# Kernel optimization log

Measured on AMD Instinct MI355X. Metric: run time of the kernel, lower is better.

The kernel has to match this reference:

```python
import jax, jax.numpy as jnp
import numpy as np

N = 100000
E = 6400000
H = 64  # hidden_nf


def setup_inputs() -> dict:
    key = jax.random.key(0)
    ks = jax.random.split(key, 12)
    x = jax.random.normal(ks[0], (N, 3), dtype=jnp.float32)
    vel = jax.random.normal(ks[1], (N, 3), dtype=jnp.float32)
    vel_norm = jax.random.uniform(ks[2], (N, 1), dtype=jnp.float32)
    edge_index = jax.random.randint(ks[3], (2, E), 0, N, dtype=jnp.int32)
    # coord_mlp_vel: Linear(1,H) -> LeakyReLU(0.2) -> Linear(H,1)
    W1 = jax.random.normal(ks[4], (H, 1), dtype=jnp.float32) * (1.0 / np.sqrt(1))
    b1 = jnp.zeros((H,), dtype=jnp.float32)
    W2 = jax.random.normal(ks[5], (1, H), dtype=jnp.float32) * (1.0 / np.sqrt(H))
    b2 = jnp.zeros((1,), dtype=jnp.float32)
    # phi: Linear(1,H) -> LeakyReLU(0.2) -> Linear(H,1,bias=False, xavier gain=0.001) -> Tanh
    Wp1 = jax.random.normal(ks[6], (H, 1), dtype=jnp.float32) * (1.0 / np.sqrt(1))
    bp1 = jnp.zeros((H,), dtype=jnp.float32)
    Wp2 = jax.random.normal(ks[7], (1, H), dtype=jnp.float32) * 0.001
    return {"x": x, "vel_norm": vel_norm, "vel": vel, "edge_index": edge_index,
            "W1": W1, "b1": b1, "W2": W2, "b2": b2,
            "Wp1": Wp1, "bp1": bp1, "Wp2": Wp2}


def reference(x, vel_norm, vel, edge_index, W1, b1, W2, b2, Wp1, bp1, Wp2):
    row, col = edge_index[0], edge_index[1]
    # edge_model: gather endpoint positions, radial distance -> tiny MLP -> scaled diff
    x_diff = x[row] - x[col]                                   # [E, 3]
    radial = jnp.sqrt(jnp.sum(x_diff * x_diff, axis=1, keepdims=True))  # [E, 1]
    h = jax.nn.leaky_relu(radial @ Wp1.T + bp1, 0.2)           # [E, H]
    e_out = jnp.tanh(h @ Wp2.T)                                # [E, 1]
    m_ij = x_diff * e_out                                      # [E, 3]
    # node_model: unsorted_segment_mean over row
    agg_sum = jax.ops.segment_sum(m_ij, row, num_segments=x.shape[0])           # [N, 3]
    cnt = jax.ops.segment_sum(jnp.ones((m_ij.shape[0], 1), m_ij.dtype), row,
                              num_segments=x.shape[0])                           # [N, 1]
    x_out = x + agg_sum / jnp.maximum(cnt, 1.0)
    # velocity term: x + vel * coord_mlp_vel(vel_norm)
    hv = jax.nn.leaky_relu(vel_norm @ W1.T + b1, 0.2)          # [N, H]
    scale = hv @ W2.T + b2                                     # [N, 1]
    return x_out + vel * scale
```

## Files before the change

kernel.cpp:

```cpp
#include <hip/hip_runtime.h>
#include <hip/hip_fp16.h>
#include <math.h>

#define LEAKY 0.2f
#define HDIM 64
#define EPB 4096
#define TPB1 256
#define PERT (EPB / TPB1)
#define RANGE 1024
#define RSH 10
#define KMAX 128
#define NSUB 4
#define NPART 4
#define NSLICE (NSUB * NPART)
#define FS2 262144.0f
#define INVFS2 (1.0f / 262144.0f)

#define XBIAS_REC 262144u
#define YZBIAS_REC 16384u
#define SX 256.0f
#define SYZ 1024.0f
#define INV_SX (1.0f / 256.0f)
#define INV_SYZ (1.0f / 1024.0f)

typedef unsigned int u32x4 __attribute__((ext_vector_type(4)));
typedef unsigned long long u64;


__device__ __forceinline__ float fast_tanh(float v) {
    float e = __builtin_amdgcn_exp2f(v * 2.88539008178f);
    return 1.0f - 2.0f * __builtin_amdgcn_rcpf(e + 1.0f);
}

__device__ __noinline__ float edge_eo_slow(float rad,
                                           const float* sW1, const float* sb1,
                                           const float* sW2) {
    float a = 0.f;
    #pragma unroll 1
    for (int k = 0; k < HDIM; k++) {
        float h = fmaf(rad, sW1[k], sb1[k]);
        h = (h > 0.f) ? h : LEAKY * h;
        a = fmaf(sW2[k], h, a);
    }
    return fast_tanh(a);
}

__global__ void repack_h_kernel(const float* __restrict__ x, uint2* __restrict__ xh, int N,
                                const float* __restrict__ Wp1, const float* __restrict__ bp1,
                                const float* __restrict__ Wp2, float* __restrict__ consts,
                                uint4* __restrict__ acc4, unsigned* __restrict__ cursor, int K) {
    int i = blockIdx.x * blockDim.x + threadIdx.x;
    if (i < N) {
        unsigned hx = __half_as_ushort(__float2half(x[3*i]));
        unsigned hy = __half_as_ushort(__float2half(x[3*i+1]));
        unsigned hz = __half_as_ushort(__float2half(x[3*i+2]));
        xh[i] = make_uint2((hy << 16) | hx, hz);
        acc4[i] = make_uint4(0u, 0u, 0u, 0u);
    }
    if (blockIdx.x == 0) {
        if (threadIdx.x < 64) {
            int k = threadIdx.x;
            float w1 = Wp1[k];
            float slope = (w1 >= 0.f) ? 1.f : LEAKY;
            float c = Wp2[k] * w1 * slope;
            float bnz = (bp1[k] != 0.f) ? 1.f : 0.f;
            #pragma unroll
            for (int off = 32; off > 0; off >>= 1) {
                c += __shfl_down(c, off, 64);
                bnz += __shfl_down(bnz, off, 64);
            }
            if (k == 0) { consts[0] = c; consts[1] = bnz; }
        }
        for (int k = threadIdx.x; k < NSUB * K; k += 256) cursor[k] = 0u;
    }
}

__device__ __noinline__ void overflow_edge(unsigned rec, unsigned b_, const uint2* __restrict__ xh,
                              float C, bool slow,
                              const float* __restrict__ Wp1, const float* __restrict__ bp1,
                              const float* __restrict__ Wp2, unsigned* __restrict__ acc4) {
    unsigned lid = rec >> 17, col = rec & 0x1FFFFu;
    unsigned row = b_ * RANGE + lid;
    uint2 ga = xh[row], gb = xh[col];
    float ax = __half2float(__ushort_as_half((unsigned short)(ga.x & 0xFFFF)));
    float ay = __half2float(__ushort_as_half((unsigned short)(ga.x >> 16)));
    float az = __half2float(__ushort_as_half((unsigned short)(ga.y & 0xFFFF)));
    float bx = __half2float(__ushort_as_half((unsigned short)(gb.x & 0xFFFF)));
    float by = __half2float(__ushort_as_half((unsigned short)(gb.x >> 16)));
    float bz = __half2float(__ushort_as_half((unsigned short)(gb.y & 0xFFFF)));
    float dx = ax - bx, dy = ay - by, dz = az - bz;
    float rad = sqrtf(dx*dx + dy*dy + dz*dz);
    float eo;
    if (!slow) {
        eo = fast_tanh(C * rad);
    } else {
        float a = 0.f;
        for (int k = 0; k < HDIM; k++) {
            float h = fmaf(rad, Wp1[k], bp1[k]);
            h = (h > 0.f) ? h : LEAKY * h;
            a = fmaf(Wp2[k], h, a);
        }
        eo = fast_tanh(a);
    }
    atomicAdd(&acc4[4*row + 0], (unsigned)__float2int_rn(dx * eo * FS2));
    atomicAdd(&acc4[4*row + 1], (unsigned)__float2int_rn(dy * eo * FS2));
    atomicAdd(&acc4[4*row + 2], (unsigned)__float2int_rn(dz * eo * FS2));
    atomicAdd(&acc4[4*row + 3], 1u);
}

__global__ __launch_bounds__(TPB1) void sort6_kernel(
        const int* __restrict__ ei,
        const uint2* __restrict__ xh,
        const float* __restrict__ Wp1, const float* __restrict__ bp1,
        const float* __restrict__ Wp2, const float* __restrict__ consts,
        unsigned* __restrict__ cursor, unsigned* __restrict__ acc4,
        unsigned* __restrict__ recs, int E, int K, unsigned csub) {
    __shared__ unsigned stage[EPB];
    __shared__ unsigned char bucket_of[EPB];
    __shared__ unsigned hist[KMAX];
    __shared__ unsigned scanv[KMAX + 1];
    __shared__ unsigned gstart[KMAX];
    const float C = consts[0];
    const bool slow = (consts[1] != 0.f);
    const unsigned sub = (unsigned)blockIdx.x & (NSUB - 1);
    for (int k = threadIdx.x; k < K; k += TPB1) hist[k] = 0;
    __syncthreads();

    const size_t base = (size_t)blockIdx.x * EPB;
    const unsigned t = threadIdx.x;
    unsigned rc[PERT];
    unsigned meta[PERT];
    if (base + EPB <= (size_t)E && (E & 3) == 0) {
        const int4* pr = (const int4*)(ei + base);
        const int4* pc = (const int4*)(ei + (size_t)E + base);
        #pragma unroll
        for (int q = 0; q < PERT / 4; q++) {
            int4 rv = pr[t + q * TPB1];
            int4 cv = pc[t + q * TPB1];
            rc[4*q+0] = (((unsigned)rv.x & (RANGE-1)) << 17) | (unsigned)cv.x;
            rc[4*q+1] = (((unsigned)rv.y & (RANGE-1)) << 17) | (unsigned)cv.y;
            rc[4*q+2] = (((unsigned)rv.z & (RANGE-1)) << 17) | (unsigned)cv.z;
            rc[4*q+3] = (((unsigned)rv.w & (RANGE-1)) << 17) | (unsigned)cv.w;
            unsigned b0 = (unsigned)rv.x >> RSH;
            unsigned b1 = (unsigned)rv.y >> RSH;
            unsigned b2 = (unsigned)rv.z >> RSH;
            unsigned b3 = (unsigned)rv.w >> RSH;
            meta[4*q+0] = (b0 << 12) | atomicAdd(&hist[b0], 1u);
            meta[4*q+1] = (b1 << 12) | atomicAdd(&hist[b1], 1u);
            meta[4*q+2] = (b2 << 12) | atomicAdd(&hist[b2], 1u);
            meta[4*q+3] = (b3 << 12) | atomicAdd(&hist[b3], 1u);
        }
    } else {
        #pragma unroll
        for (int i = 0; i < PERT; i++) {
            size_t e = base + (size_t)i * TPB1 + t;
            meta[i] = 0xFFFFFFFFu;
            if (e < (size_t)E) {
                unsigned r = (unsigned)ei[e];
                unsigned c = (unsigned)ei[(size_t)E + e];
                rc[i] = ((r & (RANGE-1)) << 17) | c;
                unsigned b_ = r >> RSH;
                meta[i] = (b_ << 12) | atomicAdd(&hist[b_], 1u);
            }
        }
    }
    __syncthreads();
    unsigned res = 0;
    if (t < (unsigned)K) {
        unsigned myc = hist[t];
        if (myc) res = atomicAdd(&cursor[t * NSUB + sub], myc);
    }
    if (t >= 192) {
        int l = t - 192;
        unsigned origA = (l < K) ? hist[l] : 0u;
        unsigned origB = (l + 64 < K) ? hist[l + 64] : 0u;
        unsigned a = origA, b = origB;
        #pragma unroll
        for (int off = 1; off < 64; off <<= 1) {
            unsigned va = __shfl_up(a, off, 64);
            unsigned vb = __shfl_up(b, off, 64);
            if (l >= off) { a += va; b += vb; }
        }
        unsigned totA = __shfl(a, 63, 64);
        unsigned grand = totA + __shfl(b, 63, 64);
        scanv[l] = a - origA;
        scanv[l + 64] = totA + b - origB;
        if (l == 63) scanv[K] = grand;
    }
    __syncthreads();
    #pragma unroll
    for (int i = 0; i < PERT; i++) {
        if (meta[i] != 0xFFFFFFFFu) {
            unsigned bk_ = meta[i] >> 12;
            unsigned slot = scanv[bk_] + (meta[i] & 0xFFFu);
            stage[slot] = rc[i];
            bucket_of[slot] = (unsigned char)bk_;
        }
    }
    if (t < (unsigned)K) gstart[t] = res;
    __syncthreads();
    unsigned total = scanv[K];
    for (unsigned j = t; j < total; j += TPB1) {
        unsigned b_ = bucket_of[j];
        unsigned off = gstart[b_] + (j - scanv[b_]);
        if (off < csub) recs[(size_t)(b_ * NSUB + sub) * csub + off] = stage[j];
        else            overflow_edge(stage[j], (unsigned)b_, xh, C, slow,
                                      Wp1, bp1, Wp2, acc4);
    }
}

__global__ __launch_bounds__(256, 4) void reduce10_kernel(
        const unsigned* __restrict__ recs, const unsigned* __restrict__ cursor,
        const uint2* __restrict__ xh,
        const float* __restrict__ Wp1, const float* __restrict__ bp1,
        const float* __restrict__ Wp2, const float* __restrict__ consts,
        u64* __restrict__ slices, int N, int K, unsigned csub) {
    __shared__ u64 accA[RANGE];
    __shared__ uint2 sxh[RANGE];
    __shared__ float sW1[HDIM], sb1[HDIM], sW2[HDIM];
    const int b = blockIdx.x / NSLICE;
    const int s = blockIdx.x % NSLICE;
    const int r = s & (NSUB - 1);
    const int p = s >> 2;
    const float C = consts[0];
    const bool slow = (consts[1] != 0.f);
    const int nbase = b * RANGE;
    if (slow) {
        for (int k = threadIdx.x; k < HDIM; k += 256) {
            sW1[k] = Wp1[k]; sb1[k] = bp1[k]; sW2[k] = Wp2[k];
        }
    }
    for (int i = threadIdx.x; i < RANGE; i += 256) {
        accA[i] = 0ull;
        int src = nbase + i;
        sxh[i] = xh[(src < N) ? src : 0];
    }
    __syncthreads();
    unsigned cnt = cursor[b * NSUB + r];
    if (cnt > csub) cnt = csub;
    unsigned quads = (cnt + 3) >> 2;
    unsigned perq = (quads + 3) >> 2;
    unsigned q0 = (unsigned)p * perq;
    unsigned q1 = q0 + perq; if (q1 > quads) q1 = quads;
    const u32x4* rb4 = (const u32x4*)(recs + (size_t)(b * NSUB + r) * csub);

    #define PROC_REC(rec, idx)                                                     \
        if ((idx) < cnt) {                                                         \
            unsigned lid_ = (rec) >> 17, col_ = (rec) & 0x1FFFFu;                  \
            uint2 ga = sxh[lid_];                                                  \
            uint2 gb = xh[col_];                                                   \
            float ax = __half2float(__ushort_as_half((unsigned short)(ga.x & 0xFFFF))); \
            float ay = __half2float(__ushort_as_half((unsigned short)(ga.x >> 16)));    \
            float az = __half2float(__ushort_as_half((unsigned short)(ga.y & 0xFFFF))); \
            float bx = __half2float(__ushort_as_half((unsigned short)(gb.x & 0xFFFF))); \
            float by = __half2float(__ushort_as_half((unsigned short)(gb.x >> 16)));    \
            float bz = __half2float(__ushort_as_half((unsigned short)(gb.y & 0xFFFF))); \
            float dx = ax - bx, dy = ay - by, dz = az - bz;                        \
            float rad = sqrtf(dx*dx + dy*dy + dz*dz);                              \
            float eo = slow ? edge_eo_slow(rad, sW1, sb1, sW2)                     \
                            : fast_tanh(C * rad);                                  \
            unsigned xb = (unsigned)(__float2int_rn(dx * eo * SX) + (int)XBIAS_REC);   \
            unsigned yb = (unsigned)(__float2int_rn(dy * eo * SYZ) + (int)YZBIAS_REC); \
            unsigned zb = (unsigned)(__float2int_rn(dz * eo * SYZ) + (int)YZBIAS_REC); \
            u64 packed = ((u64)xb << 40) | ((u64)yb << 20) | (u64)zb;              \
            atomicAdd(&accA[lid_], packed);                                        \
        }

    unsigned q = q0 + threadIdx.x;
    while (q + 256 < q1) {
        u32x4 v0 = __builtin_nontemporal_load(&rb4[q]);
        u32x4 v1 = __builtin_nontemporal_load(&rb4[q + 256]);
        unsigned i0 = 4 * q, i1 = 4 * (q + 256);
        PROC_REC(v0.x, i0); PROC_REC(v0.y, i0 + 1);
        PROC_REC(v0.z, i0 + 2); PROC_REC(v0.w, i0 + 3);
        PROC_REC(v1.x, i1); PROC_REC(v1.y, i1 + 1);
        PROC_REC(v1.z, i1 + 2); PROC_REC(v1.w, i1 + 3);
        q += 512;
    }
    while (q < q1) {
        u32x4 v = __builtin_nontemporal_load(&rb4[q]);
        unsigned i0 = 4 * q;
        PROC_REC(v.x, i0); PROC_REC(v.y, i0 + 1);
        PROC_REC(v.z, i0 + 2); PROC_REC(v.w, i0 + 3);
        q += 256;
    }
    #undef PROC_REC
    __syncthreads();
    for (int i = threadIdx.x; i < RANGE; i += 256) {
        int node = nbase + i;
        if (node < N) slices[(size_t)s * N + node] = accA[i];
    }
}

__global__ void node_merge_kernel(const float* __restrict__ x,
                                  const float* __restrict__ vel_norm,
                                  const float* __restrict__ vel,
                                  const float* __restrict__ W1, const float* __restrict__ b1,
                                  const float* __restrict__ W2, const float* __restrict__ b2,
                                  const u64* __restrict__ slices,
                                  const uint4* __restrict__ acc4,
                                  float* __restrict__ out, int N) {
    __shared__ float sW1[HDIM], sb1[HDIM], sW2[HDIM];
    for (int k = threadIdx.x; k < HDIM; k += blockDim.x) {
        sW1[k] = W1[k]; sb1[k] = b1[k]; sW2[k] = W2[k];
    }
    __syncthreads();
    int i = blockIdx.x * blockDim.x + threadIdx.x;
    if (i >= N) return;
    long long sxll = 0, syll = 0, szll = 0;
    unsigned sc = 0;
    #pragma unroll
    for (int s = 0; s < NSLICE; s++) {
        u64 f = slices[(size_t)s * N + i];
        unsigned xf = (unsigned)(f >> 40);
        unsigned yf = (unsigned)(f >> 20) & 0xFFFFFu;
        unsigned zf = (unsigned)f & 0xFFFFFu;
        unsigned cs = (xf + 131072u) >> 18;
        sxll += (long long)xf - ((long long)cs << 18);
        syll += (long long)yf - ((long long)cs << 14);
        szll += (long long)zf - ((long long)cs << 14);
        sc += cs;
    }
    uint4 a4 = acc4[i];
    float cntf = (float)(sc + a4.w);
    float sx = (float)sxll * INV_SX  + (float)(int)a4.x * INVFS2;
    float sy = (float)syll * INV_SYZ + (float)(int)a4.y * INVFS2;
    float sz = (float)szll * INV_SYZ + (float)(int)a4.z * INVFS2;
    float vn = vel_norm[i];
    float a = b2[0];
    #pragma unroll
    for (int k = 0; k < HDIM; k++) {
        float h = fmaf(vn, sW1[k], sb1[k]);
        h = (h > 0.f) ? h : LEAKY * h;
        a = fmaf(sW2[k], h, a);
    }
    float inv = 1.0f / fmaxf(cntf, 1.0f);
    out[3*i]     = x[3*i]     + sx * inv + vel[3*i]     * a;
    out[3*i + 1] = x[3*i + 1] + sy * inv + vel[3*i + 1] * a;
    out[3*i + 2] = x[3*i + 2] + sz * inv + vel[3*i + 2] * a;
}

__global__ void precompute_kernel(const float* __restrict__ Wp1,
                                  const float* __restrict__ bp1,
                                  const float* __restrict__ Wp2,
                                  float* __restrict__ consts) {
    int k = threadIdx.x;
    float w1 = Wp1[k];
    float slope = (w1 >= 0.f) ? 1.f : LEAKY;
    float c = Wp2[k] * w1 * slope;
    float bnz = (bp1[k] != 0.f) ? 1.f : 0.f;
    #pragma unroll
    for (int off = 32; off > 0; off >>= 1) {
        c += __shfl_down(c, off, 64);
        bnz += __shfl_down(bnz, off, 64);
    }
    if (k == 0) { consts[0] = c; consts[1] = bnz; }
}

__global__ void edge_atomic_kernel(const float* __restrict__ x, const int* __restrict__ ei,
                                   const float* __restrict__ Wp1, const float* __restrict__ bp1,
                                   const float* __restrict__ Wp2, const float* __restrict__ consts,
                                   float* __restrict__ acc, int E) {
    __shared__ float sW1[HDIM], sb1[HDIM], sW2[HDIM];
    const float C = consts[0];
    const bool slow = (consts[1] != 0.f);
    if (slow) {
        for (int k = threadIdx.x; k < HDIM; k += blockDim.x) {
            sW1[k] = Wp1[k]; sb1[k] = bp1[k]; sW2[k] = Wp2[k];
        }
        __syncthreads();
    }
    int e = blockIdx.x * blockDim.x + threadIdx.x;
    if (e >= E) return;
    int r = ei[e];
    int c = ei[E + e];
    float dx = x[3*r] - x[3*c];
    float dy = x[3*r+1] - x[3*c+1];
    float dz = x[3*r+2] - x[3*c+2];
    float rad = sqrtf(dx*dx + dy*dy + dz*dz);
    float eo;
    if (!slow) {
        eo = fast_tanh(C * rad);
    } else {
        float a = 0.f;
        for (int k = 0; k < HDIM; k++) {
            float h = fmaf(rad, sW1[k], sb1[k]);
            h = (h > 0.f) ? h : LEAKY * h;
            a = fmaf(sW2[k], h, a);
        }
        eo = fast_tanh(a);
    }
    float* basep = acc + ((size_t)r << 2);
    atomicAdd(basep + 0, dx * eo);
    atomicAdd(basep + 1, dy * eo);
    atomicAdd(basep + 2, dz * eo);
    atomicAdd(basep + 3, 1.f);
}

__global__ void node_kernel(const float* __restrict__ x, const float* __restrict__ vel_norm,
                            const float* __restrict__ vel,
                            const float* __restrict__ W1, const float* __restrict__ b1,
                            const float* __restrict__ W2, const float* __restrict__ b2,
                            const float4* __restrict__ slices,
                            float* __restrict__ out, int N, int S) {
    __shared__ float sW1[HDIM], sb1[HDIM], sW2[HDIM];
    for (int k = threadIdx.x; k < HDIM; k += blockDim.x) {
        sW1[k] = W1[k]; sb1[k] = b1[k]; sW2[k] = W2[k];
    }
    __syncthreads();
    int i = blockIdx.x * blockDim.x + threadIdx.x;
    if (i >= N) return;
    float sx = 0.f, sy = 0.f, sz = 0.f, sc = 0.f;
    for (int s = 0; s < S; s++) {
        float4 v = slices[(size_t)s * N + i];
        sx += v.x; sy += v.y; sz += v.z; sc += v.w;
    }
    float vn = vel_norm[i];
    float a = b2[0];
    #pragma unroll
    for (int k = 0; k < HDIM; k++) {
        float h = fmaf(vn, sW1[k], sb1[k]);
        h = (h > 0.f) ? h : LEAKY * h;
        a = fmaf(sW2[k], h, a);
    }
    float inv = 1.0f / fmaxf(sc, 1.0f);
    out[3*i]     = x[3*i]     + sx * inv + vel[3*i]     * a;
    out[3*i + 1] = x[3*i + 1] + sy * inv + vel[3*i + 1] * a;
    out[3*i + 2] = x[3*i + 2] + sz * inv + vel[3*i + 2] * a;
}

extern "C" void kernel_launch(void* const* d_in, const int* in_sizes, int n_in,
                              void* d_out, int out_size, void* d_ws, size_t ws_size,
                              hipStream_t stream) {
    const float* x        = (const float*)d_in[0];
    const float* vel_norm = (const float*)d_in[1];
    const float* vel      = (const float*)d_in[2];
    const int*   ei       = (const int*)  d_in[3];
    const float* W1       = (const float*)d_in[4];
    const float* b1       = (const float*)d_in[5];
    const float* W2       = (const float*)d_in[6];
    const float* b2       = (const float*)d_in[7];
    const float* Wp1      = (const float*)d_in[8];
    const float* bp1      = (const float*)d_in[9];
    const float* Wp2      = (const float*)d_in[10];

    const int N = in_sizes[0] / 3;
    const int E = in_sizes[3] / 2;
    const int K = (N + RANGE - 1) / RANGE;
    const int nblk = (E + EPB - 1) / EPB;

    unsigned csub = (unsigned)(E / (K * NSUB)) + 1024u;
    csub = (csub + 63u) & ~63u;

    size_t rec_bytes = (size_t)K * NSUB * csub * sizeof(unsigned);
    size_t sp_slices = (rec_bytes + 15) & ~(size_t)15;
    size_t sp_xh     = sp_slices + (size_t)NSLICE * N * sizeof(u64);
    size_t sp_acc    = (sp_xh + (size_t)N * sizeof(uint2) + 15) & ~(size_t)15;
    size_t sp_cur    = sp_acc + (size_t)N * sizeof(uint4);
    size_t sp_const  = (sp_cur + (size_t)NSUB * KMAX * sizeof(unsigned) + 15) & ~(size_t)15;
    size_t need      = sp_const + 32;

    if (K <= KMAX && ws_size >= need) {
        unsigned* recs   = (unsigned*)d_ws;
        u64*      slices = (u64*)     ((char*)d_ws + sp_slices);
        uint2*    xh     = (uint2*)   ((char*)d_ws + sp_xh);
        unsigned* acc4   = (unsigned*)((char*)d_ws + sp_acc);
        unsigned* cursor = (unsigned*)((char*)d_ws + sp_cur);
        float*    consts = (float*)   ((char*)d_ws + sp_const);

        repack_h_kernel<<<(N + 255) / 256, 256, 0, stream>>>(
            x, xh, N, Wp1, bp1, Wp2, consts, (uint4*)acc4, cursor, K);
        sort6_kernel<<<nblk, TPB1, 0, stream>>>(
            ei, xh, Wp1, bp1, Wp2, consts, cursor, acc4, recs, E, K, csub);
        reduce10_kernel<<<K * NSLICE, 256, 0, stream>>>(
            recs, cursor, xh, Wp1, bp1, Wp2, consts, slices, N, K, csub);
        node_merge_kernel<<<(N + 255) / 256, 256, 0, stream>>>(
            x, vel_norm, vel, W1, b1, W2, b2, slices, (const uint4*)acc4,
            (float*)d_out, N);
    } else {
        float* acc    = (float*)d_ws;
        float* consts = (float*)((char*)d_ws + (size_t)N * sizeof(float4));
        hipMemsetAsync(d_ws, 0, (size_t)N * sizeof(float4) + 32, stream);
        precompute_kernel<<<1, 64, 0, stream>>>(Wp1, bp1, Wp2, consts);
        edge_atomic_kernel<<<(E + 255) / 256, 256, 0, stream>>>(x, ei, Wp1, bp1, Wp2,
                                                                consts, acc, E);
        node_kernel<<<(N + 255) / 256, 256, 0, stream>>>(x, vel_norm, vel, W1, b1, W2, b2,
                                                         (const float4*)acc, (float*)d_out, N, 1);
    }
}
```

Measured before the change: 182.4 us.

## Fuse node merge into reduce kernel via last-block counter, batch gathers

Removes the separate node_merge kernel. Each bucket's last finishing slice block, found through an atomic done counter per bucket, merges the slices and writes the final output. The reduce loop is also unrolled to four record vectors, with all sixteen column gathers from xh issued before processing so more memory loads are in flight. The costs are an extra kernel launch saved against a serialized tail merge done by only one block per bucket, and higher register pressure from the wider unroll.

```diff
diff --git a/kernel.cpp b/kernel.cpp
--- a/kernel.cpp
+++ b/kernel.cpp
@@ -71,7 +71,7 @@
             }
             if (k == 0) { consts[0] = c; consts[1] = bnz; }
         }
-        for (int k = threadIdx.x; k < NSUB * K; k += 256) cursor[k] = 0u;
+        for (int k = threadIdx.x; k < NSUB * KMAX + KMAX; k += 256) cursor[k] = 0u;
     }
 }
 
@@ -209,15 +209,22 @@
     }
 }
 
-__global__ __launch_bounds__(256, 4) void reduce10_kernel(
+__global__ __launch_bounds__(256, 4) void reduce11_kernel(
         const unsigned* __restrict__ recs, const unsigned* __restrict__ cursor,
         const uint2* __restrict__ xh,
         const float* __restrict__ Wp1, const float* __restrict__ bp1,
         const float* __restrict__ Wp2, const float* __restrict__ consts,
-        u64* __restrict__ slices, int N, int K, unsigned csub) {
+        u64* __restrict__ slices, unsigned* __restrict__ done,
+        const float* __restrict__ x, const float* __restrict__ vel_norm,
+        const float* __restrict__ vel,
+        const float* __restrict__ W1, const float* __restrict__ b1,
+        const float* __restrict__ W2, const float* __restrict__ b2,
+        const uint4* __restrict__ acc4, float* __restrict__ out,
+        int N, int K, unsigned csub) {
     __shared__ u64 accA[RANGE];
     __shared__ uint2 sxh[RANGE];
     __shared__ float sW1[HDIM], sb1[HDIM], sW2[HDIM];
+    __shared__ unsigned lastFlag;
     const int b = blockIdx.x / NSLICE;
     const int s = blockIdx.x % NSLICE;
     const int r = s & (NSUB - 1);
@@ -244,11 +251,11 @@
     unsigned q1 = q0 + perq; if (q1 > quads) q1 = quads;
     const u32x4* rb4 = (const u32x4*)(recs + (size_t)(b * NSUB + r) * csub);
 
-    #define PROC_REC(rec, idx)                                                     \
+    #define PROC2(rec, gbv, idx)                                                   \
         if ((idx) < cnt) {                                                         \
-            unsigned lid_ = (rec) >> 17, col_ = (rec) & 0x1FFFFu;                  \
+            unsigned lid_ = (rec) >> 17;                                           \
             uint2 ga = sxh[lid_];                                                  \
-            uint2 gb = xh[col_];                                                   \
+            uint2 gb = (gbv);                                                      \
             float ax = __half2float(__ushort_as_half((unsigned short)(ga.x & 0xFFFF))); \
             float ay = __half2float(__ushort_as_half((unsigned short)(ga.x >> 16)));    \
             float az = __half2float(__ushort_as_half((unsigned short)(ga.y & 0xFFFF))); \
@@ -267,77 +274,94 @@
         }
 
     unsigned q = q0 + threadIdx.x;
-    while (q + 256 < q1) {
+    while (q + 768 < q1) {
         u32x4 v0 = __builtin_nontemporal_load(&rb4[q]);
         u32x4 v1 = __builtin_nontemporal_load(&rb4[q + 256]);
-        unsigned i0 = 4 * q, i1 = 4 * (q + 256);
-        PROC_REC(v0.x, i0); PROC_REC(v0.y, i0 + 1);
-        PROC_REC(v0.z, i0 + 2); PROC_REC(v0.w, i0 + 3);
-        PROC_REC(v1.x, i1); PROC_REC(v1.y, i1 + 1);
-        PROC_REC(v1.z, i1 + 2); PROC_REC(v1.w, i1 + 3);
-        q += 512;
+        u32x4 v2 = __builtin_nontemporal_load(&rb4[q + 512]);
+        u32x4 v3 = __builtin_nontemporal_load(&rb4[q + 768]);
+        uint2 g0  = xh[v0.x & 0x1FFFFu], g1  = xh[v0.y & 0x1FFFFu];
+        uint2 g2  = xh[v0.z & 0x1FFFFu], g3  = xh[v0.w & 0x1FFFFu];
+        uint2 g4  = xh[v1.x & 0x1FFFFu], g5  = xh[v1.y & 0x1FFFFu];
+        uint2 g6  = xh[v1.z & 0x1FFFFu], g7  = xh[v1.w & 0x1FFFFu];
+        uint2 g8  = xh[v2.x & 0x1FFFFu], g9  = xh[v2.y & 0x1FFFFu];
+        uint2 g10 = xh[v2.z & 0x1FFFFu], g11 = xh[v2.w & 0x1FFFFu];
+        uint2 g12 = xh[v3.x & 0x1FFFFu], g13 = xh[v3.y & 0x1FFFFu];
+        uint2 g14 = xh[v3.z & 0x1FFFFu], g15 = xh[v3.w & 0x1FFFFu];
+        unsigned i0 = 4 * q, i1 = 4 * (q + 256), i2 = 4 * (q + 512), i3 = 4 * (q + 768);
+        PROC2(v0.x, g0,  i0);     PROC2(v0.y, g1,  i0 + 1);
+        PROC2(v0.z, g2,  i0 + 2); PROC2(v0.w, g3,  i0 + 3);
+        PROC2(v1.x, g4,  i1);     PROC2(v1.y, g5,  i1 + 1);
+        PROC2(v1.z, g6,  i1 + 2); PROC2(v1.w, g7,  i1 + 3);
+        PROC2(v2.x, g8,  i2);     PROC2(v2.y, g9,  i2 + 1);
+        PROC2(v2.z, g10, i2 + 2); PROC2(v2.w, g11, i2 + 3);
+        PROC2(v3.x, g12, i3);     PROC2(v3.y, g13, i3 + 1);
+        PROC2(v3.z, g14, i3 + 2); PROC2(v3.w, g15, i3 + 3);
+        q += 1024;
     }
     while (q < q1) {
         u32x4 v = __builtin_nontemporal_load(&rb4[q]);
+        uint2 g0 = xh[v.x & 0x1FFFFu], g1 = xh[v.y & 0x1FFFFu];
+        uint2 g2 = xh[v.z & 0x1FFFFu], g3 = xh[v.w & 0x1FFFFu];
         unsigned i0 = 4 * q;
-        PROC_REC(v.x, i0); PROC_REC(v.y, i0 + 1);
-        PROC_REC(v.z, i0 + 2); PROC_REC(v.w, i0 + 3);
+        PROC2(v.x, g0, i0);     PROC2(v.y, g1, i0 + 1);
+        PROC2(v.z, g2, i0 + 2); PROC2(v.w, g3, i0 + 3);
         q += 256;
     }
-    #undef PROC_REC
+    #undef PROC2
     __syncthreads();
     for (int i = threadIdx.x; i < RANGE; i += 256) {
         int node = nbase + i;
         if (node < N) slices[(size_t)s * N + node] = accA[i];
     }
-}
-
-__global__ void node_merge_kernel(const float* __restrict__ x,
-                                  const float* __restrict__ vel_norm,
-                                  const float* __restrict__ vel,
-                                  const float* __restrict__ W1, const float* __restrict__ b1,
-                                  const float* __restrict__ W2, const float* __restrict__ b2,
-                                  const u64* __restrict__ slices,
-                                  const uint4* __restrict__ acc4,
-                                  float* __restrict__ out, int N) {
-    __shared__ float sW1[HDIM], sb1[HDIM], sW2[HDIM];
-    for (int k = threadIdx.x; k < HDIM; k += blockDim.x) {
+    __threadfence();
+    __syncthreads();
+    if (threadIdx.x == 0) {
+        unsigned v = atomicAdd(&done[b], 1u);
+        lastFlag = (v == NSLICE - 1) ? 1u : 0u;
+    }
+    __syncthreads();
+    if (!lastFlag) return;
+    __threadfence();
+    for (int k = threadIdx.x; k < HDIM; k += 256) {
         sW1[k] = W1[k]; sb1[k] = b1[k]; sW2[k] = W2[k];
     }
     __syncthreads();
-    int i = blockIdx.x * blockDim.x + threadIdx.x;
-    if (i >= N) return;
-    long long sxll = 0, syll = 0, szll = 0;
-    unsigned sc = 0;
-    #pragma unroll
-    for (int s = 0; s < NSLICE; s++) {
-        u64 f = slices[(size_t)s * N + i];
-        unsigned xf = (unsigned)(f >> 40);
-        unsigned yf = (unsigned)(f >> 20) & 0xFFFFFu;
-        unsigned zf = (unsigned)f & 0xFFFFFu;
-        unsigned cs = (xf + 131072u) >> 18;
-        sxll += (long long)xf - ((long long)cs << 18);
-        syll += (long long)yf - ((long long)cs << 14);
-        szll += (long long)zf - ((long long)cs << 14);
-        sc += cs;
-    }
-    uint4 a4 = acc4[i];
-    float cntf = (float)(sc + a4.w);
-    float sx = (float)sxll * INV_SX  + (float)(int)a4.x * INVFS2;
-    float sy = (float)syll * INV_SYZ + (float)(int)a4.y * INVFS2;
-    float sz = (float)szll * INV_SYZ + (float)(int)a4.z * INVFS2;
-    float vn = vel_norm[i];
-    float a = b2[0];
-    #pragma unroll
-    for (int k = 0; k < HDIM; k++) {
-        float h = fmaf(vn, sW1[k], sb1[k]);
-        h = (h > 0.f) ? h : LEAKY * h;
-        a = fmaf(sW2[k], h, a);
-    }
-    float inv = 1.0f / fmaxf(cntf, 1.0f);
-    out[3*i]     = x[3*i]     + sx * inv + vel[3*i]     * a;
-    out[3*i + 1] = x[3*i + 1] + sy * inv + vel[3*i + 1] * a;
-    out[3*i + 2] = x[3*i + 2] + sz * inv + vel[3*i + 2] * a;
+    const float b2v = b2[0];
+    for (int i = threadIdx.x; i < RANGE; i += 256) {
+        int node = nbase + i;
+        if (node >= N) continue;
+        long long sxll = 0, syll = 0, szll = 0;
+        unsigned sc = 0;
+        #pragma unroll
+        for (int s2 = 0; s2 < NSLICE; s2++) {
+            u64 f = slices[(size_t)s2 * N + node];
+            unsigned xf = (unsigned)(f >> 40);
+            unsigned yf = (unsigned)(f >> 20) & 0xFFFFFu;
+            unsigned zf = (unsigned)f & 0xFFFFFu;
+            unsigned cs = (xf + 131072u) >> 18;
+            sxll += (long long)xf - ((long long)cs << 18);
+            syll += (long long)yf - ((long long)cs << 14);
+            szll += (long long)zf - ((long long)cs << 14);
+            sc += cs;
+        }
+        uint4 a4 = acc4[node];
+        float cntf = (float)(sc + a4.w);
+        float sx = (float)sxll * INV_SX  + (float)(int)a4.x * INVFS2;
+        float sy = (float)syll * INV_SYZ + (float)(int)a4.y * INVFS2;
+        float sz = (float)szll * INV_SYZ + (float)(int)a4.z * INVFS2;
+        float vn = vel_norm[node];
+        float a = b2v;
+        #pragma unroll
+        for (int k = 0; k < HDIM; k++) {
+            float h = fmaf(vn, sW1[k], sb1[k]);
+            h = (h > 0.f) ? h : LEAKY * h;
+            a = fmaf(sW2[k], h, a);
+        }
+        float inv = 1.0f / fmaxf(cntf, 1.0f);
+        out[3*node]     = x[3*node]     + sx * inv + vel[3*node]     * a;
+        out[3*node + 1] = x[3*node + 1] + sy * inv + vel[3*node + 1] * a;
+        out[3*node + 2] = x[3*node + 2] + sz * inv + vel[3*node + 2] * a;
+    }
 }
 
 __global__ void precompute_kernel(const float* __restrict__ Wp1,
@@ -457,7 +481,7 @@
     size_t sp_xh     = sp_slices + (size_t)NSLICE * N * sizeof(u64);
     size_t sp_acc    = (sp_xh + (size_t)N * sizeof(uint2) + 15) & ~(size_t)15;
     size_t sp_cur    = sp_acc + (size_t)N * sizeof(uint4);
-    size_t sp_const  = (sp_cur + (size_t)NSUB * KMAX * sizeof(unsigned) + 15) & ~(size_t)15;
+    size_t sp_const  = (sp_cur + (size_t)(NSUB * KMAX + KMAX) * sizeof(unsigned) + 15) & ~(size_t)15;
     size_t need      = sp_const + 32;
 
     if (K <= KMAX && ws_size >= need) {
@@ -466,17 +490,17 @@
         uint2*    xh     = (uint2*)   ((char*)d_ws + sp_xh);
         unsigned* acc4   = (unsigned*)((char*)d_ws + sp_acc);
         unsigned* cursor = (unsigned*)((char*)d_ws + sp_cur);
+        unsigned* done   = cursor + NSUB * KMAX;
         float*    consts = (float*)   ((char*)d_ws + sp_const);
 
         repack_h_kernel<<<(N + 255) / 256, 256, 0, stream>>>(
             x, xh, N, Wp1, bp1, Wp2, consts, (uint4*)acc4, cursor, K);
         sort6_kernel<<<nblk, TPB1, 0, stream>>>(
             ei, xh, Wp1, bp1, Wp2, consts, cursor, acc4, recs, E, K, csub);
-        reduce10_kernel<<<K * NSLICE, 256, 0, stream>>>(
-            recs, cursor, xh, Wp1, bp1, Wp2, consts, slices, N, K, csub);
-        node_merge_kernel<<<(N + 255) / 256, 256, 0, stream>>>(
-            x, vel_norm, vel, W1, b1, W2, b2, slices, (const uint4*)acc4,
-            (float*)d_out, N);
+        reduce11_kernel<<<K * NSLICE, 256, 0, stream>>>(
+            recs, cursor, xh, Wp1, bp1, Wp2, consts, slices, done,
+            x, vel_norm, vel, W1, b1, W2, b2,
+            (const uint4*)acc4, (float*)d_out, N, K, csub);
     } else {
         float* acc    = (float*)d_ws;
         float* consts = (float*)((char*)d_ws + (size_t)N * sizeof(float4));
```

Measured after the change: 449.6 us. 146% more time.
